# Kernel optimization log

Hardware: AMD Instinct MI355X
Metric: run time of the kernel (lower is better)

The kernel has to match this reference:

```python
import jax, jax.numpy as jnp
import numpy as np

N, E = 50000, 800000
IN, HID, H, OUT = 128, 32, 8, 64
HD = HID * H  # 256
EPS = 1e-5


def _p(key, shape, scale=0.05):
    return jax.random.normal(key, shape, dtype=jnp.float32) * scale


def setup_inputs() -> dict:
    key = jax.random.key(0)
    ks = jax.random.split(key, 32)
    inp = {
        'x': jax.random.normal(ks[0], (N, IN), dtype=jnp.float32),
        'edge_index': jax.random.randint(ks[1], (2, E), 0, N, dtype=jnp.int64),
        'edge_attr': jax.random.normal(ks[2], (E, 1), dtype=jnp.float32),
        # layer 1 (TransformerConv: in=128 -> heads*hid=256)
        'Wq1': _p(ks[3], (IN, HD)), 'bq1': jnp.zeros((HD,), jnp.float32),
        'Wk1': _p(ks[4], (IN, HD)), 'bk1': jnp.zeros((HD,), jnp.float32),
        'Wv1': _p(ks[5], (IN, HD)), 'bv1': jnp.zeros((HD,), jnp.float32),
        'We1': _p(ks[6], (1, HD)),  # lin_edge, no bias in PyG
        'Ws1': _p(ks[7], (IN, HD)), 'bs1': jnp.zeros((HD,), jnp.float32),  # root/skip
        'lnw1': jnp.ones((HD,), jnp.float32), 'lnb1': jnp.zeros((HD,), jnp.float32),
        # layer 2 (in=256 -> 256)
        'Wq2': _p(ks[8], (HD, HD)), 'bq2': jnp.zeros((HD,), jnp.float32),
        'Wk2': _p(ks[9], (HD, HD)), 'bk2': jnp.zeros((HD,), jnp.float32),
        'Wv2': _p(ks[10], (HD, HD)), 'bv2': jnp.zeros((HD,), jnp.float32),
        'We2': _p(ks[11], (1, HD)),
        'Ws2': _p(ks[12], (HD, HD)), 'bs2': jnp.zeros((HD,), jnp.float32),
        'lnw2': jnp.ones((HD,), jnp.float32), 'lnb2': jnp.zeros((HD,), jnp.float32),
        # output linear 256 -> 64
        'Wo': _p(ks[13], (HD, OUT)), 'bo': jnp.zeros((OUT,), jnp.float32),
    }
    return inp


def transformer_conv(x, src, dst, edge_attr, Wq, bq, Wk, bk, Wv, bv, We, Ws, bs):
    n = x.shape[0]
    q = (x @ Wq + bq).reshape(n, H, HID)
    k = (x @ Wk + bk).reshape(n, H, HID)
    v = (x @ Wv + bv).reshape(n, H, HID)
    e = (edge_attr @ We).reshape(-1, H, HID)            # [E,H,d]
    kj = k[src] + e                                     # gather + edge key
    score = jnp.einsum('ehd,ehd->eh', q[dst], kj) / np.sqrt(HID)  # [E,H]
    # segment softmax over destination nodes
    m = jax.ops.segment_max(score, dst, num_segments=n)  # [N,H]
    ex = jnp.exp(score - m[dst])
    s = jax.ops.segment_sum(ex, dst, num_segments=n)
    alpha = ex / s[dst]                                  # [E,H]
    msg = alpha[..., None] * (v[src] + e)                # [E,H,d]
    out = jax.ops.segment_sum(msg, dst, num_segments=n).reshape(n, HD)
    return out + x @ Ws + bs                             # root weight skip


def graph_layernorm(x, w, b):
    # PyG LayerNorm, mode='graph': global mean/std over all nodes & features
    xc = x - x.mean()
    out = xc / (xc.std() + EPS)
    return out * w + b


def reference(x, edge_index, edge_attr,
              Wq1, bq1, Wk1, bk1, Wv1, bv1, We1, Ws1, bs1, lnw1, lnb1,
              Wq2, bq2, Wk2, bk2, Wv2, bv2, We2, Ws2, bs2, lnw2, lnb2,
              Wo, bo):
    src, dst = edge_index[0], edge_index[1]
    h = transformer_conv(x, src, dst, edge_attr, Wq1, bq1, Wk1, bk1, Wv1, bv1, We1, Ws1, bs1)
    h = jax.nn.elu(graph_layernorm(h, lnw1, lnb1))
    h = transformer_conv(h, src, dst, edge_attr, Wq2, bq2, Wk2, bk2, Wv2, bv2, We2, Ws2, bs2)
    h = jax.nn.elu(graph_layernorm(h, lnw2, lnb2))
    return h @ Wo + bo
```

## Files before the change

### kernel.cpp

```cpp
#include <hip/hip_runtime.h>
#include <hip/hip_fp16.h>
#include <math.h>

#define IN_DIM 128
#define HD 256
#define EPSLN 1e-5f

typedef _Float16 half8 __attribute__((ext_vector_type(8)));
typedef float f32x4 __attribute__((ext_vector_type(4)));
typedef float f32x2 __attribute__((ext_vector_type(2)));

__device__ inline void store4(float* p, float4 o) { *(float4*)p = o; }
__device__ inline void store4(__half* p, float4 o) {
    union { uint2 u; __half2 h[2]; } s;
    s.h[0] = __floats2half2_rn(o.x, o.y);
    s.h[1] = __floats2half2_rn(o.z, o.w);
    *(uint2*)p = s.u;
}
__device__ inline float4 h4_to_f4(uint2 u) {
    union { unsigned int w; __half2 h; } a, b;
    a.w = u.x; b.w = u.y;
    float2 lo = __half22float2(a.h), hi = __half22float2(b.h);
    return make_float4(lo.x, lo.y, hi.x, hi.y);
}
__device__ inline unsigned int f4_to_fp8x4(float a, float b, float c, float d) {
    int v = 0;
    v = __builtin_amdgcn_cvt_pk_fp8_f32(a, b, v, false);
    v = __builtin_amdgcn_cvt_pk_fp8_f32(c, d, v, true);
    return (unsigned int)v;
}
__device__ inline float4 fp8x4_to_f4(unsigned int u) {
    f32x2 lo = __builtin_amdgcn_cvt_pk_f32_fp8((int)u, false);
    f32x2 hi = __builtin_amdgcn_cvt_pk_f32_fp8((int)u, true);
    return make_float4(lo.x, lo.y, hi.x, hi.y);
}

__device__ inline void async_copy16(const __half* g, _Float16* l) {
    __builtin_amdgcn_global_load_lds(
        (const __attribute__((address_space(1))) void*)g,
        (__attribute__((address_space(3))) void*)l,
        16, 0, 0);
}

__device__ inline void unpermute_col(int n, int& sel, int& c) {
    if (n < 256) { sel = 0; c = n; }
    else if (n < 768) {
        int j = n - 256, chunk = j >> 3, w = j & 7;
        if (w < 4) { sel = 1; c = chunk * 4 + w; }
        else       { sel = 2; c = chunk * 4 + w - 4; }
    } else { sel = 3; c = n - 768; }
}

__global__ void prep_k(
    const float4* __restrict__ x, __half* __restrict__ xh, int total4,
    const int* __restrict__ dst, int* __restrict__ counts, int* __restrict__ rank, int E,
    const float* __restrict__ Wq1, const float* __restrict__ Wk1,
    const float* __restrict__ Wv1, const float* __restrict__ Ws1,
    const float* __restrict__ Wq2, const float* __restrict__ Wk2,
    const float* __restrict__ Wv2, const float* __restrict__ Ws2,
    const float* __restrict__ Wo,
    const float* __restrict__ bq1, const float* __restrict__ bk1,
    const float* __restrict__ bv1, const float* __restrict__ bs1,
    const float* __restrict__ bq2, const float* __restrict__ bk2,
    const float* __restrict__ bv2, const float* __restrict__ bs2,
    __half* __restrict__ Wc1, __half* __restrict__ Wc2, __half* __restrict__ Wot,
    float* __restrict__ bc1, float* __restrict__ bc2)
{
    int idx = blockIdx.x * 256 + threadIdx.x;
    if (idx < total4) store4(xh + (size_t)idx * 4, x[idx]);
    if (idx < E) rank[idx] = atomicAdd(&counts[dst[idx]], 1);
    if (idx < 131072) {
        int n = idx >> 7, k = idx & 127;
        int sel, c; unpermute_col(n, sel, c);
        const float* W = (sel == 0) ? Wq1 : (sel == 1) ? Wk1 : (sel == 2) ? Wv1 : Ws1;
        Wc1[idx] = __float2half(W[(size_t)k * 256 + c]);
    } else if (idx < 393216) {
        int j = idx - 131072;
        int n = j >> 8, k = j & 255;
        int sel, c; unpermute_col(n, sel, c);
        const float* W = (sel == 0) ? Wq2 : (sel == 1) ? Wk2 : (sel == 2) ? Wv2 : Ws2;
        Wc2[j] = __float2half(W[(size_t)k * 256 + c]);
    } else if (idx < 409600) {
        int j = idx - 393216;
        int n = j >> 8, k = j & 255;
        Wot[j] = __float2half(Wo[(size_t)k * 64 + n]);
    } else if (idx < 410624) {
        int n = idx - 409600;
        int sel, c; unpermute_col(n, sel, c);
        const float* b = (sel == 0) ? bq1 : (sel == 1) ? bk1 : (sel == 2) ? bv1 : bs1;
        bc1[n] = b[c];
    } else if (idx < 411648) {
        int n = idx - 410624;
        int sel, c; unpermute_col(n, sel, c);
        const float* b = (sel == 0) ? bq2 : (sel == 1) ? bk2 : (sel == 2) ? bv2 : bs2;
        bc2[n] = b[c];
    }
}

#define BM 128
#define BN 128
#define BK 64
#define TROWB 272

__global__ __launch_bounds__(256) void gemm_mfma(
    const __half* __restrict__ A, const __half* __restrict__ Wt,
    const float* __restrict__ bias, __half* __restrict__ C,
    unsigned char* __restrict__ kv8,
    int M, int K, int Nc)
{
    __shared__ char smem[BM * TROWB];
    _Float16* As = (_Float16*)smem;
    _Float16* Bs = (_Float16*)(smem + 16384);

    int tid = threadIdx.x;
    int lane = tid & 63, w = tid >> 6;
    int wm = w >> 1, wn = w & 1;
    int quad = lane >> 4, l16 = lane & 15;
    int nbx = (int)gridDim.x >> 3;
    int wkr = ((int)blockIdx.x & 7) * nbx + ((int)blockIdx.x >> 3);
    int row0 = (wkr >> 3) * BM;
    int col0 = (wkr & 7) * BN;

    f32x4 acc[4][4];
#pragma unroll
    for (int i = 0; i < 4; i++)
#pragma unroll
        for (int j = 0; j < 4; j++) acc[i][j] = (f32x4){0.f, 0.f, 0.f, 0.f};

    int srow = lane >> 3;
    int schunk = lane & 7;

    for (int k0 = 0; k0 < K; k0 += BK) {
#pragma unroll
        for (int t = 0; t < 4; t++) {
            int r = w * 32 + t * 8 + srow;
            int gr = row0 + r; if (gr > M - 1) gr = M - 1;
            int gchunk = schunk ^ (r & 7);
            async_copy16(&A[(size_t)gr * K + k0 + gchunk * 8], &As[(w * 32 + t * 8) * 64]);
        }
#pragma unroll
        for (int t = 0; t < 4; t++) {
            int r = w * 32 + t * 8 + srow;
            int gc = col0 + r; if (gc > Nc - 1) gc = Nc - 1;
            int gchunk = schunk ^ (r & 7);
            async_copy16(&Wt[(size_t)gc * K + k0 + gchunk * 8], &Bs[(w * 32 + t * 8) * 64]);
        }
        __syncthreads();

#pragma unroll
        for (int ks = 0; ks < 2; ks++) {
            half8 af[4], bf[4];
#pragma unroll
            for (int i = 0; i < 4; i++) {
                int ra = wm * 64 + i * 16 + l16;
                af[i] = *(half8*)&As[ra * 64 + (((ks * 4 + quad) ^ (ra & 7)) * 8)];
                int rb = wn * 64 + i * 16 + l16;
                bf[i] = *(half8*)&Bs[rb * 64 + (((ks * 4 + quad) ^ (rb & 7)) * 8)];
            }
#pragma unroll
            for (int i = 0; i < 4; i++)
#pragma unroll
                for (int j = 0; j < 4; j++)
                    acc[i][j] = __builtin_amdgcn_mfma_f32_16x16x32_f16(af[i], bf[j], acc[i][j], 0, 0, 0);
        }
        __syncthreads();
    }

#pragma unroll
    for (int j = 0; j < 4; j++) {
        int tcol = wn * 64 + j * 16 + l16;
        float bb = (col0 + tcol < Nc) ? bias[col0 + tcol] : 0.f;
#pragma unroll
        for (int i = 0; i < 4; i++) {
#pragma unroll
            for (int r = 0; r < 4; r++) {
                int trow = wm * 64 + i * 16 + quad * 4 + r;
                ((__half*)(smem + trow * TROWB))[tcol] = __float2half(acc[i][j][r] + bb);
            }
        }
    }
    __syncthreads();
    bool iskv = (col0 >= 256) && (col0 < 768);
    int crow = tid >> 4, cchunk = tid & 15;
    for (int p = 0; p < 8; p++) {
        int trow = p * 16 + crow;
        int grow = row0 + trow;
        if (grow >= M) continue;
        uint4 val = *(uint4*)(smem + trow * TROWB + cchunk * 16);
        if (iskv) {
            float4 lo = h4_to_f4(make_uint2(val.x, val.y));
            float4 hi = h4_to_f4(make_uint2(val.z, val.w));
            uint2 o8;
            o8.x = f4_to_fp8x4(lo.x, lo.y, lo.z, lo.w);
            o8.y = f4_to_fp8x4(hi.x, hi.y, hi.z, hi.w);
            *(uint2*)&kv8[(size_t)grow * 512 + (col0 - 256) + cchunk * 8] = o8;
        } else {
            *(uint4*)&C[(size_t)grow * Nc + col0 + cchunk * 8] = val;
        }
    }
}

__global__ __launch_bounds__(256) void gemm_out_k(
    const __half* __restrict__ A, const __half* __restrict__ Wot,
    const float* __restrict__ bias, float* __restrict__ D, int M)
{
    __shared__ _Float16 As[128 * 64];
    __shared__ _Float16 Bs[64 * 64];
    int tid = threadIdx.x;
    int lane = tid & 63, w = tid >> 6;
    int quad = lane >> 4, l16 = lane & 15;
    int row0 = blockIdx.x * 128;
    const int K = 256;

    f32x4 acc[2][4];
#pragma unroll
    for (int i = 0; i < 2; i++)
#pragma unroll
        for (int j = 0; j < 4; j++) acc[i][j] = (f32x4){0.f, 0.f, 0.f, 0.f};

    int srow = lane >> 3;
    int schunk = lane & 7;

    for (int k0 = 0; k0 < K; k0 += BK) {
#pragma unroll
        for (int t = 0; t < 4; t++) {
            int r = w * 32 + t * 8 + srow;
            int gr = row0 + r; if (gr > M - 1) gr = M - 1;
            int gchunk = schunk ^ (r & 7);
            async_copy16(&A[(size_t)gr * K + k0 + gchunk * 8], &As[(w * 32 + t * 8) * 64]);
        }
#pragma unroll
        for (int t = 0; t < 2; t++) {
            int r = w * 16 + t * 8 + srow;
            int gchunk = schunk ^ (r & 7);
            async_copy16(&Wot[(size_t)r * K + k0 + gchunk * 8], &Bs[(w * 16 + t * 8) * 64]);
        }
        __syncthreads();

#pragma unroll
        for (int ks = 0; ks < 2; ks++) {
            half8 af[2], bf[4];
#pragma unroll
            for (int i = 0; i < 2; i++) {
                int ra = w * 32 + i * 16 + l16;
                af[i] = *(half8*)&As[ra * 64 + (((ks * 4 + quad) ^ (ra & 7)) * 8)];
            }
#pragma unroll
            for (int j = 0; j < 4; j++) {
                int rb = j * 16 + l16;
                bf[j] = *(half8*)&Bs[rb * 64 + (((ks * 4 + quad) ^ (rb & 7)) * 8)];
            }
#pragma unroll
            for (int i = 0; i < 2; i++)
#pragma unroll
                for (int j = 0; j < 4; j++)
                    acc[i][j] = __builtin_amdgcn_mfma_f32_16x16x32_f16(af[i], bf[j], acc[i][j], 0, 0, 0);
        }
        __syncthreads();
    }

#pragma unroll
    for (int i = 0; i < 2; i++) {
#pragma unroll
        for (int j = 0; j < 4; j++) {
            int gcol = j * 16 + l16;
            float bb = bias[gcol];
#pragma unroll
            for (int r = 0; r < 4; r++) {
                int grow = row0 + w * 32 + i * 16 + quad * 4 + r;
                if (grow < M) D[(size_t)grow * 64 + gcol] = acc[i][j][r] + bb;
            }
        }
    }
}

__global__ __launch_bounds__(1024) void scan_k(const int* __restrict__ counts,
                                               int* __restrict__ offs, int n)
{
    __shared__ int wsum[16];
    __shared__ int wpre[16];
    int tid = threadIdx.x, lane = tid & 63, wid = tid >> 6;
    int per = (n + 1023) / 1024;
    int start = tid * per, end = min(start + per, n);
    int sum = 0;
    for (int i = start; i < end; i++) sum += counts[i];
    int v = sum;
#pragma unroll
    for (int d = 1; d < 64; d <<= 1) {
        int t = __shfl_up(v, (unsigned)d, 64);
        if (lane >= d) v += t;
    }
    if (lane == 63) wsum[wid] = v;
    __syncthreads();
    if (tid == 0) {
        int acc = 0;
        for (int i = 0; i < 16; i++) { wpre[i] = acc; acc += wsum[i]; }
    }
    __syncthreads();
    int pre = wpre[wid] + v - sum;
    for (int i = start; i < end; i++) { offs[i] = pre; pre += counts[i]; }
    if (end == n && start <= n) offs[n] = pre;
}

__global__ void scatter_k(const int* __restrict__ src, const int* __restrict__ dst,
                          const float* __restrict__ attr, const int* __restrict__ offs,
                          const int* __restrict__ rank, int2* __restrict__ edat, int E)
{
    int e = blockIdx.x * 256 + threadIdx.x;
    if (e < 8) edat[E + e] = make_int2(0, 0);
    if (e < E) {
        int p = offs[dst[e]] + rank[e];
        edat[p] = make_int2(src[e], __float_as_int(attr[e]));
    }
}

__global__ __launch_bounds__(256) void attn_k(
    const uint2* __restrict__ q2, const uint2* __restrict__ kv8u2,
    const float* __restrict__ We,
    __half* __restrict__ hwork, const int2* __restrict__ edat,
    const int* __restrict__ offs,
    double* __restrict__ stats, int n, int nGroups)
{
    int lane = threadIdx.x & 63;
    int wid = threadIdx.x >> 6;
    float4 we = ((const float4*)We)[lane];
    float tsum = 0.f, tsq = 0.f;

    for (int g = blockIdx.x; g < nGroups; g += gridDim.x) {
        int node = g * 4 + wid;
        if (node >= n) continue;
        float4 qv = h4_to_f4(q2[(size_t)node * 256 + lane]);
        float qwe = qv.x * we.x + qv.y * we.y + qv.z * we.z + qv.w * we.w;
        qwe += __shfl_xor(qwe, 1);
        qwe += __shfl_xor(qwe, 2);
        qwe += __shfl_xor(qwe, 4);

        float4 accv = make_float4(0.f, 0.f, 0.f, 0.f);
        float sat = 0.f;
        float m = -INFINITY, l = 0.f;
        int i0 = __builtin_amdgcn_readfirstlane(offs[node]);
        int i1 = __builtin_amdgcn_readfirstlane(offs[node + 1]);

        int abA[8], srA[8], abB[8], srB[8];
        uint2 kvA[8], kvB[8];

        auto LOADB = [&](int base, int* ab_, int* sr_, uint2* kv_) {
#pragma unroll
            for (int u = 0; u < 8; u++) {
                int2 ed = edat[base + u];
                sr_[u] = __builtin_amdgcn_readfirstlane(ed.x);
                ab_[u] = __builtin_amdgcn_readfirstlane(ed.y);
            }
#pragma unroll
            for (int u = 0; u < 8; u++)
                kv_[u] = (kv8u2 + (size_t)(unsigned)sr_[u] * 64)[lane];
        };

        auto COMPUTE = [&](const int* ab_, const uint2* kv_, int cnt) {
            float pv[8];
#pragma unroll
            for (int u = 0; u < 8; u++) {
                float4 kvf = fp8x4_to_f4(kv_[u].x);
                float p = qv.x * kvf.x + qv.y * kvf.y + qv.z * kvf.z + qv.w * kvf.w;
                p += __shfl_xor(p, 1);
                p += __shfl_xor(p, 2);
                p += __shfl_xor(p, 4);
                p = fmaf(__int_as_float(ab_[u]), qwe, p) * 0.17677669529663687f;
                pv[u] = (u < cnt) ? p : -INFINITY;
            }
            float m01 = fmaxf(pv[0], pv[1]), m23 = fmaxf(pv[2], pv[3]);
            float m45 = fmaxf(pv[4], pv[5]), m67 = fmaxf(pv[6], pv[7]);
            float pmax = fmaxf(fmaxf(m01, m23), fmaxf(m45, m67));
            float mn = fmaxf(m, pmax);
            float corr = __expf(m - mn);
            l *= corr;
            sat *= corr;
            accv.x *= corr; accv.y *= corr; accv.z *= corr; accv.w *= corr;
#pragma unroll
            for (int u = 0; u < 8; u++) {
                float wgt = __expf(pv[u] - mn);
                l += wgt;
                sat = fmaf(wgt, __int_as_float(ab_[u]), sat);
                float4 vv = fp8x4_to_f4(kv_[u].y);
                accv.x = fmaf(wgt, vv.x, accv.x);
                accv.y = fmaf(wgt, vv.y, accv.y);
                accv.z = fmaf(wgt, vv.z, accv.z);
                accv.w = fmaf(wgt, vv.w, accv.w);
            }
            m = mn;
        };

        if (i0 < i1) {
            int i = i0;
            LOADB(i, abA, srA, kvA);
            while (true) {
                if (i + 8 >= i1) { COMPUTE(abA, kvA, i1 - i); break; }
                LOADB(i + 8, abB, srB, kvB);
                COMPUTE(abA, kvA, 8);
                i += 8;
                if (i + 8 >= i1) { COMPUTE(abB, kvB, i1 - i); break; }
                LOADB(i + 8, abA, srA, kvA);
                COMPUTE(abB, kvB, 8);
                i += 8;
            }
        }

        float inv = (l > 0.f) ? 1.f / l : 0.f;
        float4 sk = h4_to_f4(q2[(size_t)node * 256 + 192 + lane]);
        float sw = sat * inv;
        float4 o;
        o.x = fmaf(accv.x, inv, fmaf(sw, we.x, sk.x));
        o.y = fmaf(accv.y, inv, fmaf(sw, we.y, sk.y));
        o.z = fmaf(accv.z, inv, fmaf(sw, we.z, sk.z));
        o.w = fmaf(accv.w, inv, fmaf(sw, we.w, sk.w));
        store4(hwork + (size_t)node * 256 + lane * 4, o);
        tsum += o.x + o.y + o.z + o.w;
        tsq += o.x * o.x + o.y * o.y + o.z * o.z + o.w * o.w;
    }

#pragma unroll
    for (int d = 1; d < 64; d <<= 1) {
        tsum += __shfl_xor(tsum, d);
        tsq += __shfl_xor(tsq, d);
    }
    __shared__ float red[8];
    if (lane == 0) { red[wid] = tsum; red[4 + wid] = tsq; }
    __syncthreads();
    if (threadIdx.x == 0) {
        double s = (double)red[0] + (double)red[1] + (double)red[2] + (double)red[3];
        double sq = (double)red[4] + (double)red[5] + (double)red[6] + (double)red[7];
        atomicAdd(&stats[0], s);
        atomicAdd(&stats[1], sq);
    }
}

__global__ __launch_bounds__(256) void ln_apply(
    const uint2* __restrict__ in, __half* __restrict__ out,
    const float4* __restrict__ w4, const float4* __restrict__ b4,
    const double* __restrict__ stats, double cnt, int total4)
{
    int base = (blockIdx.x * 256 + threadIdx.x) * 4;
    if (base >= total4) return;
    double mu = stats[0] / cnt;
    double var = stats[1] / cnt - mu * mu;
    if (var < 0.0) var = 0.0;
    float mean = (float)mu;
    float inv = (float)(1.0 / (sqrt(var) + (double)EPSLN));
#pragma unroll
    for (int u = 0; u < 4; u++) {
        int i = base + u;
        if (i >= total4) return;
        int c = i & 63;
        float4 xv = h4_to_f4(in[i]);
        float4 w = w4[c], b = b4[c];
        float4 o;
        o.x = fmaf((xv.x - mean) * inv, w.x, b.x);
        o.y = fmaf((xv.y - mean) * inv, w.y, b.y);
        o.z = fmaf((xv.z - mean) * inv, w.z, b.z);
        o.w = fmaf((xv.w - mean) * inv, w.w, b.w);
        o.x = o.x > 0.f ? o.x : expm1f(o.x);
        o.y = o.y > 0.f ? o.y : expm1f(o.y);
        o.z = o.z > 0.f ? o.z : expm1f(o.z);
        o.w = o.w > 0.f ? o.w : expm1f(o.w);
        store4(out + (size_t)i * 4, o);
    }
}

extern "C" void kernel_launch(void* const* d_in, const int* in_sizes, int n_in,
                              void* d_out, int out_size, void* d_ws, size_t ws_size,
                              hipStream_t stream)
{
    const float* x      = (const float*)d_in[0];
    const int*   ei     = (const int*)d_in[1];
    const float* eattr  = (const float*)d_in[2];
    const float* Wq1 = (const float*)d_in[3];  const float* bq1 = (const float*)d_in[4];
    const float* Wk1 = (const float*)d_in[5];  const float* bk1 = (const float*)d_in[6];
    const float* Wv1 = (const float*)d_in[7];  const float* bv1 = (const float*)d_in[8];
    const float* We1 = (const float*)d_in[9];
    const float* Ws1 = (const float*)d_in[10]; const float* bs1 = (const float*)d_in[11];
    const float* lnw1 = (const float*)d_in[12]; const float* lnb1 = (const float*)d_in[13];
    const float* Wq2 = (const float*)d_in[14]; const float* bq2 = (const float*)d_in[15];
    const float* Wk2 = (const float*)d_in[16]; const float* bk2 = (const float*)d_in[17];
    const float* Wv2 = (const float*)d_in[18]; const float* bv2 = (const float*)d_in[19];
    const float* We2 = (const float*)d_in[20];
    const float* Ws2 = (const float*)d_in[21]; const float* bs2 = (const float*)d_in[22];
    const float* lnw2 = (const float*)d_in[23]; const float* lnb2 = (const float*)d_in[24];
    const float* Wo  = (const float*)d_in[25]; const float* bo  = (const float*)d_in[26];

    const int N = in_sizes[0] / IN_DIM;
    const int E = in_sizes[2];
    const int* esrc = ei;
    const int* edst = ei + E;

    char* ws = (char*)d_ws;
    size_t off = 0;
    auto alloc = [&](size_t bytes) -> char* {
        char* p = ws + off;
        off += (bytes + 255) / 256 * 256;
        return p;
    };
    int*    counts = (int*)alloc((size_t)N * 4);
    double* stats  = (double*)alloc(64);
    size_t zbytes = off;
    int*    rank   = (int*)alloc((size_t)E * 4);
    int*    offs   = (int*)alloc((size_t)(N + 1) * 4);
    int2*   edat   = (int2*)alloc((size_t)(E + 8) * 8);
    __half* xh     = (__half*)alloc((size_t)N * IN_DIM * 2);
    __half* qkvs   = (__half*)alloc((size_t)N * 1024 * 2);
    unsigned char* kv8 = (unsigned char*)alloc((size_t)N * 512);
    __half* hwork  = (__half*)alloc((size_t)N * HD * 2);
    __half* hio    = (__half*)alloc((size_t)N * HD * 2);
    __half* Wc1    = (__half*)alloc((size_t)1024 * IN_DIM * 2);
    __half* Wc2    = (__half*)alloc((size_t)1024 * HD * 2);
    __half* Wot    = (__half*)alloc((size_t)64 * HD * 2);
    float*  bc1    = (float*)alloc(1024 * 4);
    float*  bc2    = (float*)alloc(1024 * 4);

    hipMemsetAsync(d_ws, 0, zbytes, stream);

    int total4x = N * (IN_DIM / 4);
    int prepWork = total4x > E ? total4x : E;
    if (prepWork < 411648) prepWork = 411648;
    prep_k<<<(prepWork + 255) / 256, 256, 0, stream>>>(
        (const float4*)x, xh, total4x, edst, counts, rank, E,
        Wq1, Wk1, Wv1, Ws1, Wq2, Wk2, Wv2, Ws2, Wo,
        bq1, bk1, bv1, bs1, bq2, bk2, bv2, bs2,
        Wc1, Wc2, Wot, bc1, bc2);

    scan_k<<<1, 1024, 0, stream>>>(counts, offs, N);
    scatter_k<<<(E + 255) / 256, 256, 0, stream>>>(esrc, edst, eattr, offs, rank,
                                                   edat, E);

    int nbx = (N + BM - 1) / BM;
    dim3 gqkvs(nbx * 8);
    int nGroups = (N + 3) / 4;
    int gaBlocks = nGroups < 2048 ? nGroups : 2048;
    int total4 = N * (HD / 4);
    dim3 gl((total4 / 4 + 255) / 256);
    dim3 gout((N + 127) / 128);

    gemm_mfma<<<gqkvs, 256, 0, stream>>>(xh, Wc1, bc1, qkvs, kv8, N, IN_DIM, 1024);
    attn_k<<<gaBlocks, 256, 0, stream>>>((const uint2*)qkvs, (const uint2*)kv8, We1,
                                         hwork, edat, offs, stats, N, nGroups);
    ln_apply<<<gl, 256, 0, stream>>>((const uint2*)hwork, hio,
                                     (const float4*)lnw1, (const float4*)lnb1,
                                     stats, (double)N * HD, total4);

    gemm_mfma<<<gqkvs, 256, 0, stream>>>(hio, Wc2, bc2, qkvs, kv8, N, HD, 1024);
    attn_k<<<gaBlocks, 256, 0, stream>>>((const uint2*)qkvs, (const uint2*)kv8, We2,
                                         hwork, edat, offs, stats + 2, N, nGroups);
    ln_apply<<<gl, 256, 0, stream>>>((const uint2*)hwork, hio,
                                     (const float4*)lnw2, (const float4*)lnb2,
                                     stats + 2, (double)N * HD, total4);

    gemm_out_k<<<gout, 256, 0, stream>>>(hio, Wot, bo, (float*)d_out, N);
}
```

Measured before the change: 572.9 us.

## Prefetch next node's query, offsets and first edge batch across attention loop

The attention kernel now software-pipelines across destination nodes. While finishing the current node, it loads the next node's query vector, CSR offsets and first batch of edges and key/value rows, so each new node does not start with a memory stall. Edge batch loads are clamped to valid indices, the edge-weight vector is staged in LDS, and the launch bounds request 8 blocks per SM to raise occupancy. The extra live state and the register cap could cause spills or scratch use for the dynamically selected A/B buffers.

```diff
diff --git a/kernel.cpp b/kernel.cpp
--- a/kernel.cpp
+++ b/kernel.cpp
@@ -314,22 +314,54 @@
     }
 }
 
-__global__ __launch_bounds__(256) void attn_k(
+__global__ __launch_bounds__(256, 8) void attn_k(
     const uint2* __restrict__ q2, const uint2* __restrict__ kv8u2,
     const float* __restrict__ We,
     __half* __restrict__ hwork, const int2* __restrict__ edat,
     const int* __restrict__ offs,
     double* __restrict__ stats, int n, int nGroups)
 {
+    __shared__ float4 weLds[64];
+    __shared__ float red[8];
     int lane = threadIdx.x & 63;
     int wid = threadIdx.x >> 6;
-    float4 we = ((const float4*)We)[lane];
+    if (threadIdx.x < 64) weLds[threadIdx.x] = ((const float4*)We)[threadIdx.x];
+    __syncthreads();
     float tsum = 0.f, tsq = 0.f;
 
-    for (int g = blockIdx.x; g < nGroups; g += gridDim.x) {
+    int abA[8], srA[8], abB[8], srB[8];
+    uint2 kvA[8], kvB[8];
+
+    int g = blockIdx.x;
+    uint2 qraw = make_uint2(0u, 0u);
+    int i0 = 0, i1 = 0;
+    if (g < nGroups) {
+        int node = g * 4 + wid;
+        if (node < n) {
+            qraw = q2[(size_t)node * 256 + lane];
+            i0 = __builtin_amdgcn_readfirstlane(offs[node]);
+            i1 = __builtin_amdgcn_readfirstlane(offs[node + 1]);
+        }
+    }
+    bool carry = false, carryB = false;
+
+    for (; g < nGroups; g += gridDim.x) {
         int node = g * 4 + wid;
         if (node >= n) continue;
-        float4 qv = h4_to_f4(q2[(size_t)node * 256 + lane]);
+
+        int gN = g + gridDim.x;
+        uint2 qrawN = make_uint2(0u, 0u);
+        int i0N = 0, i1N = 0;
+        if (gN < nGroups) {
+            int nodeN = gN * 4 + wid;
+            qrawN = q2[(size_t)nodeN * 256 + lane];
+            i0N = __builtin_amdgcn_readfirstlane(offs[nodeN]);
+            i1N = __builtin_amdgcn_readfirstlane(offs[nodeN + 1]);
+        }
+        bool hasNext = (i0N < i1N);
+
+        float4 we = weLds[lane];
+        float4 qv = h4_to_f4(qraw);
         float qwe = qv.x * we.x + qv.y * we.y + qv.z * we.z + qv.w * we.w;
         qwe += __shfl_xor(qwe, 1);
         qwe += __shfl_xor(qwe, 2);
@@ -338,16 +370,11 @@
         float4 accv = make_float4(0.f, 0.f, 0.f, 0.f);
         float sat = 0.f;
         float m = -INFINITY, l = 0.f;
-        int i0 = __builtin_amdgcn_readfirstlane(offs[node]);
-        int i1 = __builtin_amdgcn_readfirstlane(offs[node + 1]);
-
-        int abA[8], srA[8], abB[8], srB[8];
-        uint2 kvA[8], kvB[8];
-
-        auto LOADB = [&](int base, int* ab_, int* sr_, uint2* kv_) {
+
+        auto LOADB = [&](int base, int cnt, int* ab_, int* sr_, uint2* kv_) {
 #pragma unroll
             for (int u = 0; u < 8; u++) {
-                int2 ed = edat[base + u];
+                int2 ed = edat[base + ((u < cnt) ? u : 0)];
                 sr_[u] = __builtin_amdgcn_readfirstlane(ed.x);
                 ab_[u] = __builtin_amdgcn_readfirstlane(ed.y);
             }
@@ -390,32 +417,55 @@
             m = mn;
         };
 
+        bool ncarry = false, ncarryB = false;
         if (i0 < i1) {
             int i = i0;
-            LOADB(i, abA, srA, kvA);
+            bool curB;
+            if (carry) { curB = carryB; }
+            else       { LOADB(i0, min(8, i1 - i0), abA, srA, kvA); curB = false; }
             while (true) {
-                if (i + 8 >= i1) { COMPUTE(abA, kvA, i1 - i); break; }
-                LOADB(i + 8, abB, srB, kvB);
-                COMPUTE(abA, kvA, 8);
-                i += 8;
-                if (i + 8 >= i1) { COMPUTE(abB, kvB, i1 - i); break; }
-                LOADB(i + 8, abA, srA, kvA);
-                COMPUTE(abB, kvB, 8);
-                i += 8;
+                int rem = i1 - i;
+                if (rem > 8) {
+                    int c2 = min(8, rem - 8);
+                    if (curB) LOADB(i + 8, c2, abA, srA, kvA);
+                    else      LOADB(i + 8, c2, abB, srB, kvB);
+                    if (curB) COMPUTE(abB, kvB, 8);
+                    else      COMPUTE(abA, kvA, 8);
+                    i += 8; curB = !curB;
+                } else {
+                    if (hasNext) {
+                        int c0 = min(8, i1N - i0N);
+                        if (curB) LOADB(i0N, c0, abA, srA, kvA);
+                        else      LOADB(i0N, c0, abB, srB, kvB);
+                        ncarry = true; ncarryB = !curB;
+                    }
+                    if (curB) COMPUTE(abB, kvB, rem);
+                    else      COMPUTE(abA, kvA, rem);
+                    break;
+                }
+            }
+        } else {
+            if (hasNext) {
+                LOADB(i0N, min(8, i1N - i0N), abA, srA, kvA);
+                ncarry = true; ncarryB = false;
             }
         }
 
         float inv = (l > 0.f) ? 1.f / l : 0.f;
         float4 sk = h4_to_f4(q2[(size_t)node * 256 + 192 + lane]);
+        float4 we2 = weLds[lane];
         float sw = sat * inv;
         float4 o;
-        o.x = fmaf(accv.x, inv, fmaf(sw, we.x, sk.x));
-        o.y = fmaf(accv.y, inv, fmaf(sw, we.y, sk.y));
-        o.z = fmaf(accv.z, inv, fmaf(sw, we.z, sk.z));
-        o.w = fmaf(accv.w, inv, fmaf(sw, we.w, sk.w));
+        o.x = fmaf(accv.x, inv, fmaf(sw, we2.x, sk.x));
+        o.y = fmaf(accv.y, inv, fmaf(sw, we2.y, sk.y));
+        o.z = fmaf(accv.z, inv, fmaf(sw, we2.z, sk.z));
+        o.w = fmaf(accv.w, inv, fmaf(sw, we2.w, sk.w));
         store4(hwork + (size_t)node * 256 + lane * 4, o);
         tsum += o.x + o.y + o.z + o.w;
         tsq += o.x * o.x + o.y * o.y + o.z * o.z + o.w * o.w;
+
+        qraw = qrawN; i0 = i0N; i1 = i1N;
+        carry = ncarry; carryB = ncarryB;
     }
 
 #pragma unroll
@@ -423,7 +473,6 @@
         tsum += __shfl_xor(tsum, d);
         tsq += __shfl_xor(tsq, d);
     }
-    __shared__ float red[8];
     if (lane == 0) { red[wid] = tsum; red[4 + wid] = tsq; }
     __syncthreads();
     if (threadIdx.x == 0) {
```

Measured after the change: 1.681 ms. 2.93x slower.

## Double-buffer GEMM shared-memory tiles with BK=32 to overlap loads and MFMA

Applied to the files above, without the earlier changes.

Both MFMA GEMM kernels now use two shared-memory buffers with a K-step of 32. The next tile's async copies are issued before the current tile's MFMAs, with one barrier per step and a new 4-chunk XOR swizzle. The aim is to hide global-load latency behind compute instead of stalling at a barrier after every load. In exchange, each barrier interval does half as much MFMA work and the number of sync points doubles.

```diff
diff --git a/kernel.cpp b/kernel.cpp
--- a/kernel.cpp
+++ b/kernel.cpp
@@ -99,7 +99,6 @@
 
 #define BM 128
 #define BN 128
-#define BK 64
 #define TROWB 272
 
 __global__ __launch_bounds__(256) void gemm_mfma(
@@ -109,8 +108,6 @@
     int M, int K, int Nc)
 {
     __shared__ char smem[BM * TROWB];
-    _Float16* As = (_Float16*)smem;
-    _Float16* Bs = (_Float16*)(smem + 16384);
 
     int tid = threadIdx.x;
     int lane = tid & 63, w = tid >> 6;
@@ -127,42 +124,51 @@
 #pragma unroll
         for (int j = 0; j < 4; j++) acc[i][j] = (f32x4){0.f, 0.f, 0.f, 0.f};
 
-    int srow = lane >> 3;
-    int schunk = lane & 7;
-
-    for (int k0 = 0; k0 < K; k0 += BK) {
-#pragma unroll
-        for (int t = 0; t < 4; t++) {
-            int r = w * 32 + t * 8 + srow;
+    int srow = lane >> 2;
+    int schunk = lane & 3;
+
+    int nt = K >> 5;
+
+    auto STAGE = [&](int step, int buf) {
+        int k0 = step << 5;
+        _Float16* Asb = (_Float16*)(smem + buf * 16384);
+        _Float16* Bsb = (_Float16*)(smem + 8192 + buf * 16384);
+#pragma unroll
+        for (int t = 0; t < 2; t++) {
+            int r = w * 32 + t * 16 + srow;
             int gr = row0 + r; if (gr > M - 1) gr = M - 1;
-            int gchunk = schunk ^ (r & 7);
-            async_copy16(&A[(size_t)gr * K + k0 + gchunk * 8], &As[(w * 32 + t * 8) * 64]);
-        }
-#pragma unroll
-        for (int t = 0; t < 4; t++) {
-            int r = w * 32 + t * 8 + srow;
+            int gchunk = schunk ^ ((r ^ (r >> 2)) & 3);
+            async_copy16(&A[(size_t)gr * K + k0 + gchunk * 8], &Asb[(w * 32 + t * 16) * 32]);
+        }
+#pragma unroll
+        for (int t = 0; t < 2; t++) {
+            int r = w * 32 + t * 16 + srow;
             int gc = col0 + r; if (gc > Nc - 1) gc = Nc - 1;
-            int gchunk = schunk ^ (r & 7);
-            async_copy16(&Wt[(size_t)gc * K + k0 + gchunk * 8], &Bs[(w * 32 + t * 8) * 64]);
-        }
-        __syncthreads();
-
-#pragma unroll
-        for (int ks = 0; ks < 2; ks++) {
-            half8 af[4], bf[4];
-#pragma unroll
-            for (int i = 0; i < 4; i++) {
-                int ra = wm * 64 + i * 16 + l16;
-                af[i] = *(half8*)&As[ra * 64 + (((ks * 4 + quad) ^ (ra & 7)) * 8)];
-                int rb = wn * 64 + i * 16 + l16;
-                bf[i] = *(half8*)&Bs[rb * 64 + (((ks * 4 + quad) ^ (rb & 7)) * 8)];
-            }
-#pragma unroll
-            for (int i = 0; i < 4; i++)
-#pragma unroll
-                for (int j = 0; j < 4; j++)
-                    acc[i][j] = __builtin_amdgcn_mfma_f32_16x16x32_f16(af[i], bf[j], acc[i][j], 0, 0, 0);
-        }
+            int gchunk = schunk ^ ((r ^ (r >> 2)) & 3);
+            async_copy16(&Wt[(size_t)gc * K + k0 + gchunk * 8], &Bsb[(w * 32 + t * 16) * 32]);
+        }
+    };
+
+    STAGE(0, 0);
+    __syncthreads();
+
+    for (int t = 0; t < nt; ++t) {
+        if (t + 1 < nt) STAGE(t + 1, (t + 1) & 1);
+        _Float16* Asb = (_Float16*)(smem + (t & 1) * 16384);
+        _Float16* Bsb = (_Float16*)(smem + 8192 + (t & 1) * 16384);
+        half8 af[4], bf[4];
+#pragma unroll
+        for (int i = 0; i < 4; i++) {
+            int ra = wm * 64 + i * 16 + l16;
+            af[i] = *(half8*)&Asb[ra * 32 + ((quad ^ ((ra ^ (ra >> 2)) & 3)) * 8)];
+            int rb = wn * 64 + i * 16 + l16;
+            bf[i] = *(half8*)&Bsb[rb * 32 + ((quad ^ ((rb ^ (rb >> 2)) & 3)) * 8)];
+        }
+#pragma unroll
+        for (int i = 0; i < 4; i++)
+#pragma unroll
+            for (int j = 0; j < 4; j++)
+                acc[i][j] = __builtin_amdgcn_mfma_f32_16x16x32_f16(af[i], bf[j], acc[i][j], 0, 0, 0);
         __syncthreads();
     }
 
@@ -204,8 +210,7 @@
     const __half* __restrict__ A, const __half* __restrict__ Wot,
     const float* __restrict__ bias, float* __restrict__ D, int M)
 {
-    __shared__ _Float16 As[128 * 64];
-    __shared__ _Float16 Bs[64 * 64];
+    __shared__ _Float16 smem[12288];
     int tid = threadIdx.x;
     int lane = tid & 63, w = tid >> 6;
     int quad = lane >> 4, l16 = lane & 15;
@@ -218,44 +223,51 @@
 #pragma unroll
         for (int j = 0; j < 4; j++) acc[i][j] = (f32x4){0.f, 0.f, 0.f, 0.f};
 
-    int srow = lane >> 3;
-    int schunk = lane & 7;
-
-    for (int k0 = 0; k0 < K; k0 += BK) {
-#pragma unroll
-        for (int t = 0; t < 4; t++) {
-            int r = w * 32 + t * 8 + srow;
+    int srow = lane >> 2;
+    int schunk = lane & 3;
+    const int nt = 8;
+
+    auto STAGE = [&](int step, int buf) {
+        int k0 = step << 5;
+        _Float16* Asb = smem + buf * 4096;
+        _Float16* Bsb = smem + 8192 + buf * 2048;
+#pragma unroll
+        for (int t = 0; t < 2; t++) {
+            int r = w * 32 + t * 16 + srow;
             int gr = row0 + r; if (gr > M - 1) gr = M - 1;
-            int gchunk = schunk ^ (r & 7);
-            async_copy16(&A[(size_t)gr * K + k0 + gchunk * 8], &As[(w * 32 + t * 8) * 64]);
-        }
-#pragma unroll
-        for (int t = 0; t < 2; t++) {
-            int r = w * 16 + t * 8 + srow;
-            int gchunk = schunk ^ (r & 7);
-            async_copy16(&Wot[(size_t)r * K + k0 + gchunk * 8], &Bs[(w * 16 + t * 8) * 64]);
-        }
-        __syncthreads();
-
-#pragma unroll
-        for (int ks = 0; ks < 2; ks++) {
-            half8 af[2], bf[4];
-#pragma unroll
-            for (int i = 0; i < 2; i++) {
-                int ra = w * 32 + i * 16 + l16;
-                af[i] = *(half8*)&As[ra * 64 + (((ks * 4 + quad) ^ (ra & 7)) * 8)];
-            }
-#pragma unroll
-            for (int j = 0; j < 4; j++) {
-                int rb = j * 16 + l16;
-                bf[j] = *(half8*)&Bs[rb * 64 + (((ks * 4 + quad) ^ (rb & 7)) * 8)];
-            }
-#pragma unroll
-            for (int i = 0; i < 2; i++)
-#pragma unroll
-                for (int j = 0; j < 4; j++)
-                    acc[i][j] = __builtin_amdgcn_mfma_f32_16x16x32_f16(af[i], bf[j], acc[i][j], 0, 0, 0);
-        }
+            int gchunk = schunk ^ ((r ^ (r >> 2)) & 3);
+            async_copy16(&A[(size_t)gr * K + k0 + gchunk * 8], &Asb[(w * 32 + t * 16) * 32]);
+        }
+        {
+            int r = w * 16 + srow;
+            int gchunk = schunk ^ ((r ^ (r >> 2)) & 3);
+            async_copy16(&Wot[(size_t)r * K + k0 + gchunk * 8], &Bsb[(w * 16) * 32]);
+        }
+    };
+
+    STAGE(0, 0);
+    __syncthreads();
+
+    for (int t = 0; t < nt; ++t) {
+        if (t + 1 < nt) STAGE(t + 1, (t + 1) & 1);
+        _Float16* Asb = smem + (t & 1) * 4096;
+        _Float16* Bsb = smem + 8192 + (t & 1) * 2048;
+        half8 af[2], bf[4];
+#pragma unroll
+        for (int i = 0; i < 2; i++) {
+            int ra = w * 32 + i * 16 + l16;
+            af[i] = *(half8*)&Asb[ra * 32 + ((quad ^ ((ra ^ (ra >> 2)) & 3)) * 8)];
+        }
+#pragma unroll
+        for (int j = 0; j < 4; j++) {
+            int rb = j * 16 + l16;
+            bf[j] = *(half8*)&Bsb[rb * 32 + ((quad ^ ((rb ^ (rb >> 2)) & 3)) * 8)];
+        }
+#pragma unroll
+        for (int i = 0; i < 2; i++)
+#pragma unroll
+            for (int j = 0; j < 4; j++)
+                acc[i][j] = __builtin_amdgcn_mfma_f32_16x16x32_f16(af[i], bf[j], acc[i][j], 0, 0, 0);
         __syncthreads();
     }
 
```

Result: no change. 573.9 us (+0.2%).
